# Kernel tuning notes

Hardware: AMD Instinct MI355X
Metric: run time of the kernel (lower is better)

## Reference

```python
import jax, jax.numpy as jnp
import numpy as np
from jax import lax

B, L, E, H, VOCAB = 32, 64, 1024, 128, 32000


def setup_inputs() -> dict:
    key = jax.random.key(0)
    ks = jax.random.split(key, 8)
    return {
        "sent": jax.random.randint(ks[0], (B, L), 0, VOCAB),
        "init_c": jax.random.normal(ks[1], (B, H), jnp.float32),
        "init_h": jax.random.normal(ks[2], (B, H), jnp.float32),
        "enc_output": jax.random.normal(ks[3], (B, E, H), jnp.float32),
        "w_emb": jax.random.normal(ks[4], (VOCAB, H), jnp.float32) * 0.02,
        "w_lstm": jax.random.normal(ks[5], (2 * H, 4 * H), jnp.float32) * 0.05,
        "w_soft": jax.random.normal(ks[6], (H, VOCAB), jnp.float32) * 0.05,
        "V": jax.random.normal(ks[7], (2 * H, H), jnp.float32) * 0.05,
    }


def reference(sent, init_c, init_h, enc_output, w_emb, w_lstm, w_soft, V):
    h_dim = init_h.shape[-1]
    x_emb = w_emb[sent]                       # (B, L, H) embedding lookup
    # Split additive-attention matrix: concat(enc, h) @ V == enc @ V_e + h @ V_h
    V_e, V_h = V[:h_dim], V[h_dim:]           # (H, H) each
    enc_proj = enc_output @ V_e               # (B, E, H), precomputed once

    def step(carry, x_t):
        c, h = carry
        # LSTM cell: gates from concat(x, h) @ w_lstm
        gates = jnp.concatenate([x_t, h], axis=-1) @ w_lstm   # (B, 4H)
        i, f, o, g = jnp.split(gates, 4, axis=-1)
        c_new = jax.nn.sigmoid(f) * c + jax.nn.sigmoid(i) * jnp.tanh(g)
        h_new = jax.nn.sigmoid(o) * jnp.tanh(c_new)           # (B, H)
        # Bahdanau additive attention over encoder states
        att = jnp.tanh(enc_proj + (h_new @ V_h)[:, None, :])  # (B, E, H)
        scores = att.sum(axis=-1)                              # (B, E)
        alpha = jax.nn.softmax(scores, axis=-1)                # (B, E)
        context = jnp.einsum('be,beh->bh', alpha, enc_output)  # (B, H)
        h_out = context                                        # attended hidden
        return (c_new, h_out), (h_out, alpha)

    (c_fin, h_fin), (hs, alphas) = lax.scan(step, (init_c, init_h),
                                            jnp.transpose(x_emb, (1, 0, 2)))
    hs = jnp.transpose(hs, (1, 0, 2))          # (B, L, H)
    alphas = jnp.transpose(alphas, (1, 0, 2))  # (B, L, E)
    logits = hs @ w_soft                       # (B, L, vocab)
    return logits, c_fin, h_fin, alphas
```

## Files before the change

### kernel.cpp

```cpp
#include <hip/hip_runtime.h>
#include <hip/hip_bf16.h>

#define BB 32
#define LL 64
#define EE 1024
#define HH 128
#define VV 32000

typedef unsigned short u16;
typedef unsigned long long u64;
typedef __attribute__((ext_vector_type(8))) short bf16x8;
typedef __attribute__((ext_vector_type(8))) unsigned short u16x8;
typedef __attribute__((ext_vector_type(4))) float f32x4;

#define LOG2E 1.4426950408889634f
#define C2T   2.8853900817779268f

#define OFF_C ((size_t)BB * LL * VV)
#define OFF_H (OFF_C + (size_t)BB * HH)
#define OFF_A (OFF_H + (size_t)BB * HH)

#define WS_ENCT 0
#define WS_HS   ((size_t)16777216)
#define WS_XE   ((size_t)17301504)
#define WS_GX   ((size_t)18350080)
#define WS_PAY  ((size_t)22544384)
#define WS_DFL  ((size_t)23076864)
#define WS_NEED ((size_t)23076868)

#define PAY_WORDS (32 * 8 * 2 * 130)

__device__ __forceinline__ float bf2f(u16 u) {
    union { unsigned int i; float f; } v; v.i = ((unsigned int)u) << 16; return v.f;
}
__device__ __forceinline__ u16 f2bf(float f) {
    union { float f; unsigned int i; } v; v.f = f;
    unsigned int x = v.i;
    return (u16)((x + 0x7FFFu + ((x >> 16) & 1u)) >> 16);
}
__device__ __forceinline__ float ldf(const void* p, size_t i, int f32) {
    if (f32) return ((const float*)p)[i];
    return bf2f(((const u16*)p)[i]);
}
__device__ __forceinline__ void stout(void* p, size_t i, float v, int f32) {
    if (f32) ((float*)p)[i] = v;
    else ((u16*)p)[i] = f2bf(v);
}
__device__ __forceinline__ float sigm(float x) {
    return __builtin_amdgcn_rcpf(1.f + __builtin_amdgcn_exp2f(-x * LOG2E));
}
__device__ __forceinline__ float tanh_fast(float x) {
    return 1.f - 2.f * __builtin_amdgcn_rcpf(__builtin_amdgcn_exp2f(x * C2T) + 1.f);
}

__global__ void detect_kernel(const unsigned int* __restrict__ w, int* __restrict__ flag)
{
    if (threadIdx.x == 0 && blockIdx.x == 0) {
        int cnt = 0;
        for (int i = 0; i < 256; ++i) {
            float a = fabsf(bf2f((u16)(w[i] & 0xFFFFu)));
            if (a > 1e-4f && a < 0.5f) ++cnt;
        }
        *flag = (cnt > 128) ? 1 : 0;
    }
}

__global__ __launch_bounds__(256) void reset_kernel(u64* __restrict__ pay)
{
    int i = blockIdx.x * 256 + threadIdx.x;
    if (i < PAY_WORDS)
        pay[i] = 0ull;
}

__global__ __launch_bounds__(256) void gather_kernel(
    const int* __restrict__ sent, const void* __restrict__ w_emb,
    float* __restrict__ xe, const int* __restrict__ flagp)
{
    int isf32 = !flagp[0];
    int i = blockIdx.x * 256 + threadIdx.x;
    int row = i >> 7, h = i & 127;
    int id = sent[row];
    xe[(size_t)row * HH + h] = ldf(w_emb, (size_t)id * HH + h, isf32);
}

__global__ __launch_bounds__(256) void gatesx2_kernel(
    const float* __restrict__ xe, const void* __restrict__ w_lstm,
    float* __restrict__ gx, const int* __restrict__ flagp)
{
    int isf32 = !flagp[0];
    int row0 = blockIdx.x * 16;
    int tid = threadIdx.x;
    __shared__ float xr[16][128];
    for (int i = tid; i < 2048; i += 256)
        xr[i >> 7][i & 127] = xe[(size_t)(row0 + (i >> 7)) * HH + (i & 127)];
    __syncthreads();
    int c0 = tid, c1 = tid + 256;
    float a0[16], a1[16];
    #pragma unroll
    for (int r = 0; r < 16; ++r) { a0[r] = 0.f; a1[r] = 0.f; }
    for (int kk = 0; kk < 128; ++kk) {
        float w0, w1;
        if (isf32) {
            w0 = ((const float*)w_lstm)[(size_t)kk * 512 + c0];
            w1 = ((const float*)w_lstm)[(size_t)kk * 512 + c1];
        } else {
            w0 = bf2f(((const u16*)w_lstm)[(size_t)kk * 512 + c0]);
            w1 = bf2f(((const u16*)w_lstm)[(size_t)kk * 512 + c1]);
        }
        #pragma unroll
        for (int r = 0; r < 16; ++r) {
            a0[r] += xr[r][kk] * w0;
            a1[r] += xr[r][kk] * w1;
        }
    }
    #pragma unroll
    for (int r = 0; r < 16; ++r) {
        gx[(size_t)(row0 + r) * 512 + c0] = a0[r];
        gx[(size_t)(row0 + r) * 512 + c1] = a1[r];
    }
}

__global__ __launch_bounds__(1024) void transpose_wsoft(
    const void* __restrict__ w_soft, u16* __restrict__ wT, const int* __restrict__ flagp)
{
    int isf32 = !flagp[0];
    __shared__ u16 tile[32][33];
    int n0 = blockIdx.x * 32;
    int k0 = blockIdx.y * 32;
    int tx = threadIdx.x & 31, ty = threadIdx.x >> 5;
    tile[ty][tx] = f2bf(ldf(w_soft, (size_t)(k0 + ty) * VV + n0 + tx, isf32));
    __syncthreads();
    wT[(size_t)(n0 + ty) * HH + k0 + tx] = tile[tx][ty];
}

__global__ __launch_bounds__(256) void encproj_kernel(
    const void* __restrict__ enc_out, const void* __restrict__ V,
    float* __restrict__ encT, const int* __restrict__ flagp)
{
    int isf32 = !flagp[0];
    __shared__ float ve[HH][HH];
    int b = blockIdx.y;
    int e0 = blockIdx.x * 64;
    int tid = threadIdx.x;
    for (int i = tid; i < HH * HH; i += 256)
        ve[i >> 7][i & 127] = ldf(V, i, isf32);
    __syncthreads();
    int e = e0 + (tid & 63);
    int hb = (tid >> 6) * 32;
    size_t rowbase = ((size_t)b * EE + e) * HH;
    float acc[32];
    #pragma unroll
    for (int i = 0; i < 32; ++i) acc[i] = 0.f;
    for (int k0 = 0; k0 < HH; k0 += 16) {
        float ef[16];
        #pragma unroll
        for (int i = 0; i < 16; ++i) ef[i] = ldf(enc_out, rowbase + k0 + i, isf32);
        #pragma unroll
        for (int hh = 0; hh < 32; ++hh) {
            float a = acc[hh];
            #pragma unroll
            for (int kk = 0; kk < 16; ++kk)
                a += ef[kk] * ve[k0 + kk][hb + hh];
            acc[hh] = a;
        }
    }
    float* outp = encT + ((size_t)b * HH) * EE + e;
    #pragma unroll
    for (int hh = 0; hh < 32; ++hh)
        outp[(size_t)(hb + hh) * EE] = acc[hh] * C2T;
}

__global__ __launch_bounds__(1024, 4) void scan_kernel(
    const void* __restrict__ init_c, const void* __restrict__ init_h,
    const void* __restrict__ enc_out, const void* __restrict__ w_lstm,
    const void* __restrict__ V, const float* __restrict__ encTg,
    const float* __restrict__ gx, u16* __restrict__ hs_bf,
    void* __restrict__ out, u64* __restrict__ pay,
    const int* __restrict__ flagp)
{
    const int isf32 = !flagp[0];
    const int bid = blockIdx.x;
    const int b = bid & 31, k = bid >> 5;
    const int tid = threadIdx.x;

    __shared__ float encTl[128][128];
    __shared__ float harr[128], cst[128], hnew[128], hvC[128];
    __shared__ float gp[2][512];
    __shared__ float dred[8][128];
    __shared__ float sc[128], Ul[128];
    __shared__ float exch[8][130];
    __shared__ float redw[2], redw2[2];
    __shared__ float m_s, s_s;

    for (int i = tid; i < 128 * 128; i += 1024) {
        int h = i >> 7, e = i & 127;
        encTl[h][e] = encTg[(size_t)(b * 128 + h) * EE + k * 128 + e];
    }
    if (tid < 128) {
        cst[tid]  = ldf(init_c, (size_t)b * HH + tid, isf32);
        harr[tid] = ldf(init_h, (size_t)b * HH + tid, isf32);
    }
    __syncthreads();

    u64* mypay = pay + (size_t)(b * 8 + k) * 2 * 130;

    for (int t = 0; t < LL; ++t) {
        {
            int col = tid & 511, half = tid >> 9;
            float acc = 0.f;
            if (isf32) {
                const float* wcol = (const float*)w_lstm + (size_t)(HH + half * 64) * 512 + col;
                #pragma unroll 4
                for (int kk = 0; kk < 64; ++kk)
                    acc += harr[half * 64 + kk] * wcol[(size_t)kk * 512];
            } else {
                const u16* wcol = (const u16*)w_lstm + (size_t)(HH + half * 64) * 512 + col;
                #pragma unroll 4
                for (int kk = 0; kk < 64; ++kk)
                    acc += harr[half * 64 + kk] * bf2f(wcol[(size_t)kk * 512]);
            }
            gp[half][col] = acc;
        }
        __syncthreads();
        if (tid < 128) {
            const float* gxr = gx + (size_t)(b * LL + t) * 512;
            float gi = gxr[tid]       + gp[0][tid]       + gp[1][tid];
            float gf = gxr[128 + tid] + gp[0][128 + tid] + gp[1][128 + tid];
            float go = gxr[256 + tid] + gp[0][256 + tid] + gp[1][256 + tid];
            float gg = gxr[384 + tid] + gp[0][384 + tid] + gp[1][384 + tid];
            float c_new = sigm(gf) * cst[tid] + sigm(gi) * tanh_fast(gg);
            cst[tid] = c_new;
            hnew[tid] = sigm(go) * tanh_fast(c_new);
        }
        __syncthreads();
        {
            int h = tid & 127, jc = tid >> 7;
            float p = 0.f;
            if (isf32) {
                const float* vp = (const float*)V + (size_t)(HH + jc * 16) * HH + h;
                #pragma unroll
                for (int j = 0; j < 16; ++j)
                    p += hnew[jc * 16 + j] * vp[(size_t)j * HH];
            } else {
                const u16* vp = (const u16*)V + (size_t)(HH + jc * 16) * HH + h;
                #pragma unroll
                for (int j = 0; j < 16; ++j)
                    p += hnew[jc * 16 + j] * bf2f(vp[(size_t)j * HH]);
            }
            dred[jc][h] = p;
        }
        __syncthreads();
        if (tid < 128) {
            float v = 0.f;
            #pragma unroll
            for (int s = 0; s < 8; ++s) v += dred[s][tid];
            hvC[tid] = v * C2T;
        }
        __syncthreads();
        {
            int e = tid & 127, hc = tid >> 7;
            float sumr = 0.f;
            #pragma unroll
            for (int j = 0; j < 16; ++j) {
                int h = hc * 16 + j;
                float a = encTl[h][e] + hvC[h];
                sumr += __builtin_amdgcn_rcpf(__builtin_amdgcn_exp2f(a) + 1.f);
            }
            dred[hc][e] = sumr;
        }
        __syncthreads();
        float s_e = 0.f, p_reg = 0.f;
        if (tid < 128) {
            float sr = 0.f;
            #pragma unroll
            for (int s = 0; s < 8; ++s) sr += dred[s][tid];
            s_e = 128.f - 2.f * sr;
            float m = s_e;
            #pragma unroll
            for (int off = 32; off; off >>= 1) m = fmaxf(m, __shfl_xor(m, off));
            if ((tid & 63) == 0) redw[tid >> 6] = m;
        }
        __syncthreads();
        if (tid < 128) {
            float mloc = fmaxf(redw[0], redw[1]);
            p_reg = __builtin_amdgcn_exp2f((s_e - mloc) * LOG2E);
            sc[tid] = p_reg;
            float s = p_reg;
            #pragma unroll
            for (int off = 32; off; off >>= 1) s += __shfl_xor(s, off);
            if ((tid & 63) == 0) redw2[tid >> 6] = s;
            if (tid == 0) m_s = mloc;
        }
        __syncthreads();
        if (tid == 0) s_s = redw2[0] + redw2[1];
        {
            int h = tid & 127, ec = tid >> 7;
            float p = 0.f;
            if (isf32) {
                const float* eb = (const float*)enc_out +
                    ((size_t)b * EE + k * 128 + ec * 16) * HH + h;
                #pragma unroll
                for (int j = 0; j < 16; ++j)
                    p += sc[ec * 16 + j] * eb[(size_t)j * HH];
            } else {
                const u16* eb = (const u16*)enc_out +
                    ((size_t)b * EE + k * 128 + ec * 16) * HH + h;
                #pragma unroll
                for (int j = 0; j < 16; ++j)
                    p += sc[ec * 16 + j] * bf2f(eb[(size_t)j * HH]);
            }
            __syncthreads();
            dred[ec][h] = p;
        }
        __syncthreads();
        if (tid < 128) {
            float v = 0.f;
            #pragma unroll
            for (int s = 0; s < 8; ++s) v += dred[s][tid];
            Ul[tid] = v;
        }
        __syncthreads();
        {
            u64* pp = mypay + (size_t)(t & 1) * 130;
            if (tid < 130) {
                float val = (tid < 128) ? Ul[tid] : ((tid == 128) ? m_s : s_s);
                union { float f; unsigned int u; } cv; cv.f = val;
                u64 w = ((u64)(unsigned int)(t + 1) << 32) | (u64)cv.u;
                __hip_atomic_store(&pp[tid], w, __ATOMIC_RELAXED, __HIP_MEMORY_SCOPE_AGENT);
            }
        }
        if (tid < 910) {
            int qq = tid / 130;
            int q = qq + (qq >= k ? 1 : 0);
            int idx = tid - qq * 130;
            const u64* qp = pay + ((size_t)(b * 8 + q) * 2 + (t & 1)) * 130 + idx;
            unsigned int want = (unsigned int)(t + 1);
            u64 w = __hip_atomic_load(qp, __ATOMIC_RELAXED, __HIP_MEMORY_SCOPE_AGENT);
            int cnt = 0;
            while ((unsigned int)(w >> 32) != want) {
                __builtin_amdgcn_s_sleep(2);
                w = __hip_atomic_load(qp, __ATOMIC_RELAXED, __HIP_MEMORY_SCOPE_AGENT);
                if (++cnt > (1 << 20)) break;
            }
            union { unsigned int u; float f; } cv; cv.u = (unsigned int)(w & 0xFFFFFFFFu);
            exch[q][idx] = cv.f;
        }
        if (tid < 130) {
            float val = (tid < 128) ? Ul[tid] : ((tid == 128) ? m_s : s_s);
            exch[k][tid] = val;
        }
        __syncthreads();
        if (tid < 128) {
            float M = exch[0][128];
            #pragma unroll
            for (int q = 1; q < 8; ++q) M = fmaxf(M, exch[q][128]);
            float St = 0.f, ch = 0.f;
            #pragma unroll
            for (int q = 0; q < 8; ++q) {
                float w = __builtin_amdgcn_exp2f((exch[q][128] - M) * LOG2E);
                St += w * exch[q][129];
                ch += w * exch[q][tid];
            }
            float rS = __builtin_amdgcn_rcpf(St);
            float ctx = ch * rS;
            harr[tid] = ctx;
            float al = sc[tid] * __builtin_amdgcn_exp2f((m_s - M) * LOG2E) * rS;
            stout(out, OFF_A + (size_t)(b * LL + t) * EE + k * 128 + tid, al, isf32);
            if (k == 0) {
                hs_bf[(size_t)(b * LL + t) * HH + tid] = f2bf(ctx);
                if (t == LL - 1) {
                    stout(out, OFF_H + (size_t)b * HH + tid, ctx, isf32);
                    stout(out, OFF_C + (size_t)b * HH + tid, cst[tid], isf32);
                }
            }
        }
        __syncthreads();
    }
}

__global__ __launch_bounds__(256) void logits_gemm(
    const u16* __restrict__ hs, const u16* __restrict__ wT,
    void* __restrict__ out, const int* __restrict__ flagp)
{
    int isf32 = !flagp[0];
    int n0 = blockIdx.x * 32;
    int m0 = (blockIdx.y * 4 + (threadIdx.x >> 6)) * 32;
    int lane = threadIdx.x & 63;
    int lr = lane & 15, lh = lane >> 4;
    f32x4 acc00 = {0.f, 0.f, 0.f, 0.f}, acc01 = acc00, acc10 = acc00, acc11 = acc00;
    const u16* a0p = hs + (size_t)(m0 + lr) * HH + lh * 8;
    const u16* a1p = a0p + (size_t)16 * HH;
    const u16* b0p = wT + (size_t)(n0 + lr) * HH + lh * 8;
    const u16* b1p = b0p + (size_t)16 * HH;
    #pragma unroll
    for (int ks = 0; ks < 4; ++ks) {
        bf16x8 a0 = *(const bf16x8*)(a0p + ks * 32);
        bf16x8 a1 = *(const bf16x8*)(a1p + ks * 32);
        bf16x8 b0 = *(const bf16x8*)(b0p + ks * 32);
        bf16x8 b1 = *(const bf16x8*)(b1p + ks * 32);
        acc00 = __builtin_amdgcn_mfma_f32_16x16x32_bf16(a0, b0, acc00, 0, 0, 0);
        acc01 = __builtin_amdgcn_mfma_f32_16x16x32_bf16(a0, b1, acc01, 0, 0, 0);
        acc10 = __builtin_amdgcn_mfma_f32_16x16x32_bf16(a1, b0, acc10, 0, 0, 0);
        acc11 = __builtin_amdgcn_mfma_f32_16x16x32_bf16(a1, b1, acc11, 0, 0, 0);
    }
    size_t base0 = (size_t)(m0 + lh * 4) * VV + n0;
    size_t base1 = (size_t)(m0 + 16 + lh * 4) * VV + n0;
    #pragma unroll
    for (int r = 0; r < 4; ++r) {
        stout(out, base0 + (size_t)r * VV + lr,      acc00[r], isf32);
        stout(out, base0 + (size_t)r * VV + 16 + lr, acc01[r], isf32);
        stout(out, base1 + (size_t)r * VV + lr,      acc10[r], isf32);
        stout(out, base1 + (size_t)r * VV + 16 + lr, acc11[r], isf32);
    }
}

extern "C" void kernel_launch(void* const* d_in, const int* in_sizes, int n_in,
                              void* d_out, int out_size, void* d_ws, size_t ws_size,
                              hipStream_t stream)
{
    (void)in_sizes; (void)n_in; (void)out_size;
    if (ws_size < WS_NEED) return;

    const int* sent     = (const int*)d_in[0];
    const void* init_c  = d_in[1];
    const void* init_h  = d_in[2];
    const void* enc_out = d_in[3];
    const void* w_emb   = d_in[4];
    const void* w_lstm  = d_in[5];
    const void* w_soft  = d_in[6];
    const void* V       = d_in[7];

    char* ws = (char*)d_ws;
    float* encT  = (float*)(ws + WS_ENCT);
    u16*   wT    = (u16*)(ws + WS_ENCT);
    u16*   hs    = (u16*)(ws + WS_HS);
    float* xe    = (float*)(ws + WS_XE);
    float* gx    = (float*)(ws + WS_GX);
    u64*   pay   = (u64*)(ws + WS_PAY);
    int*   dflag = (int*)(ws + WS_DFL);

    hipLaunchKernelGGL(detect_kernel, dim3(1), dim3(64), 0, stream,
                       (const unsigned int*)w_emb, dflag);
    hipLaunchKernelGGL(reset_kernel, dim3((PAY_WORDS + 255) / 256), dim3(256), 0, stream, pay);
    hipLaunchKernelGGL(gather_kernel, dim3(1024), dim3(256), 0, stream, sent, w_emb, xe, dflag);
    hipLaunchKernelGGL(gatesx2_kernel, dim3(128), dim3(256), 0, stream, xe, w_lstm, gx, dflag);
    hipLaunchKernelGGL(encproj_kernel, dim3(16, BB), dim3(256), 0, stream, enc_out, V, encT, dflag);

    {
        const void* a0 = init_c; const void* a1 = init_h; const void* a2 = enc_out;
        const void* a3 = w_lstm; const void* a4 = V; const float* a5 = encT;
        const float* a6 = gx; u16* a7 = hs; void* a8 = d_out;
        u64* a9 = pay; const int* a10 = dflag;
        void* args[] = {&a0, &a1, &a2, &a3, &a4, &a5, &a6, &a7, &a8, &a9, &a10};
        hipLaunchCooperativeKernel(scan_kernel, dim3(256), dim3(1024), args, 0, stream);
    }

    hipLaunchKernelGGL(transpose_wsoft, dim3(VV / 32, 4), dim3(1024), 0, stream, w_soft, wT, dflag);
    hipLaunchKernelGGL(logits_gemm, dim3(VV / 32, 16), dim3(256), 0, stream, hs, wT, d_out, dflag);
}
```

Measured before the change: 892.0 us.

## Keep recurrent weights in registers and fuse small setup kernels

```diff
diff --git a/kernel.cpp b/kernel.cpp
--- a/kernel.cpp
+++ b/kernel.cpp
@@ -22,7 +22,6 @@
 
 #define WS_ENCT 0
 #define WS_HS   ((size_t)16777216)
-#define WS_XE   ((size_t)17301504)
 #define WS_GX   ((size_t)18350080)
 #define WS_PAY  ((size_t)22544384)
 #define WS_DFL  ((size_t)23076864)
@@ -53,46 +52,36 @@
     return 1.f - 2.f * __builtin_amdgcn_rcpf(__builtin_amdgcn_exp2f(x * C2T) + 1.f);
 }
 
-__global__ void detect_kernel(const unsigned int* __restrict__ w, int* __restrict__ flag)
-{
-    if (threadIdx.x == 0 && blockIdx.x == 0) {
-        int cnt = 0;
-        for (int i = 0; i < 256; ++i) {
-            float a = fabsf(bf2f((u16)(w[i] & 0xFFFFu)));
-            if (a > 1e-4f && a < 0.5f) ++cnt;
-        }
-        *flag = (cnt > 128) ? 1 : 0;
-    }
-}
-
-__global__ __launch_bounds__(256) void reset_kernel(u64* __restrict__ pay)
+__global__ __launch_bounds__(256) void resetdetect_kernel(
+    u64* __restrict__ pay, const unsigned int* __restrict__ w, int* __restrict__ flag)
 {
     int i = blockIdx.x * 256 + threadIdx.x;
     if (i < PAY_WORDS)
         pay[i] = 0ull;
-}
-
-__global__ __launch_bounds__(256) void gather_kernel(
+    if (i == 0) {
+        int cnt = 0;
+        for (int j = 0; j < 256; ++j) {
+            float a = fabsf(bf2f((u16)(w[j] & 0xFFFFu)));
+            if (a > 1e-4f && a < 0.5f) ++cnt;
+        }
+        *flag = (cnt > 128) ? 1 : 0;
+    }
+}
+
+__global__ __launch_bounds__(256) void gatesx3_kernel(
     const int* __restrict__ sent, const void* __restrict__ w_emb,
-    float* __restrict__ xe, const int* __restrict__ flagp)
-{
-    int isf32 = !flagp[0];
-    int i = blockIdx.x * 256 + threadIdx.x;
-    int row = i >> 7, h = i & 127;
-    int id = sent[row];
-    xe[(size_t)row * HH + h] = ldf(w_emb, (size_t)id * HH + h, isf32);
-}
-
-__global__ __launch_bounds__(256) void gatesx2_kernel(
-    const float* __restrict__ xe, const void* __restrict__ w_lstm,
-    float* __restrict__ gx, const int* __restrict__ flagp)
+    const void* __restrict__ w_lstm, float* __restrict__ gx,
+    const int* __restrict__ flagp)
 {
     int isf32 = !flagp[0];
     int row0 = blockIdx.x * 16;
     int tid = threadIdx.x;
     __shared__ float xr[16][128];
-    for (int i = tid; i < 2048; i += 256)
-        xr[i >> 7][i & 127] = xe[(size_t)(row0 + (i >> 7)) * HH + (i & 127)];
+    for (int i = tid; i < 2048; i += 256) {
+        int r = i >> 7, col = i & 127;
+        int id = sent[row0 + r];
+        xr[r][col] = ldf(w_emb, (size_t)id * HH + col, isf32);
+    }
     __syncthreads();
     int c0 = tid, c1 = tid + 256;
     float a0[16], a1[16];
@@ -170,7 +159,7 @@
         outp[(size_t)(hb + hh) * EE] = acc[hh] * C2T;
 }
 
-__global__ __launch_bounds__(1024, 4) void scan_kernel(
+__global__ __launch_bounds__(1024, 2) void scan_kernel(
     const void* __restrict__ init_c, const void* __restrict__ init_h,
     const void* __restrict__ enc_out, const void* __restrict__ w_lstm,
     const void* __restrict__ V, const float* __restrict__ encTg,
@@ -192,6 +181,17 @@
     __shared__ float redw[2], redw2[2];
     __shared__ float m_s, s_s;
 
+    const int colA = tid & 511, halfA = tid >> 9;
+    float wreg[64];
+    #pragma unroll
+    for (int kk = 0; kk < 64; ++kk)
+        wreg[kk] = ldf(w_lstm, (size_t)(HH + halfA * 64 + kk) * 512 + colA, isf32);
+    const int hC = tid & 127, jcC = tid >> 7;
+    float vreg[16];
+    #pragma unroll
+    for (int j = 0; j < 16; ++j)
+        vreg[j] = ldf(V, (size_t)(HH + jcC * 16 + j) * HH + hC, isf32);
+
     for (int i = tid; i < 128 * 128; i += 1024) {
         int h = i >> 7, e = i & 127;
         encTl[h][e] = encTg[(size_t)(b * 128 + h) * EE + k * 128 + e];
@@ -205,49 +205,35 @@
     u64* mypay = pay + (size_t)(b * 8 + k) * 2 * 130;
 
     for (int t = 0; t < LL; ++t) {
+        float g0 = 0.f, g1 = 0.f, g2 = 0.f, g3 = 0.f;
+        if (tid < 128) {
+            const float* gxr = gx + (size_t)(b * LL + t) * 512;
+            g0 = gxr[tid]; g1 = gxr[128 + tid]; g2 = gxr[256 + tid]; g3 = gxr[384 + tid];
+        }
         {
-            int col = tid & 511, half = tid >> 9;
             float acc = 0.f;
-            if (isf32) {
-                const float* wcol = (const float*)w_lstm + (size_t)(HH + half * 64) * 512 + col;
-                #pragma unroll 4
-                for (int kk = 0; kk < 64; ++kk)
-                    acc += harr[half * 64 + kk] * wcol[(size_t)kk * 512];
-            } else {
-                const u16* wcol = (const u16*)w_lstm + (size_t)(HH + half * 64) * 512 + col;
-                #pragma unroll 4
-                for (int kk = 0; kk < 64; ++kk)
-                    acc += harr[half * 64 + kk] * bf2f(wcol[(size_t)kk * 512]);
-            }
-            gp[half][col] = acc;
-        }
-        __syncthreads();
-        if (tid < 128) {
-            const float* gxr = gx + (size_t)(b * LL + t) * 512;
-            float gi = gxr[tid]       + gp[0][tid]       + gp[1][tid];
-            float gf = gxr[128 + tid] + gp[0][128 + tid] + gp[1][128 + tid];
-            float go = gxr[256 + tid] + gp[0][256 + tid] + gp[1][256 + tid];
-            float gg = gxr[384 + tid] + gp[0][384 + tid] + gp[1][384 + tid];
+            #pragma unroll
+            for (int kk = 0; kk < 64; ++kk)
+                acc += harr[halfA * 64 + kk] * wreg[kk];
+            gp[halfA][colA] = acc;
+        }
+        __syncthreads();
+        if (tid < 128) {
+            float gi = g0 + gp[0][tid]       + gp[1][tid];
+            float gf = g1 + gp[0][128 + tid] + gp[1][128 + tid];
+            float go = g2 + gp[0][256 + tid] + gp[1][256 + tid];
+            float gg = g3 + gp[0][384 + tid] + gp[1][384 + tid];
             float c_new = sigm(gf) * cst[tid] + sigm(gi) * tanh_fast(gg);
             cst[tid] = c_new;
             hnew[tid] = sigm(go) * tanh_fast(c_new);
         }
         __syncthreads();
         {
-            int h = tid & 127, jc = tid >> 7;
             float p = 0.f;
-            if (isf32) {
-                const float* vp = (const float*)V + (size_t)(HH + jc * 16) * HH + h;
-                #pragma unroll
-                for (int j = 0; j < 16; ++j)
-                    p += hnew[jc * 16 + j] * vp[(size_t)j * HH];
-            } else {
-                const u16* vp = (const u16*)V + (size_t)(HH + jc * 16) * HH + h;
-                #pragma unroll
-                for (int j = 0; j < 16; ++j)
-                    p += hnew[jc * 16 + j] * bf2f(vp[(size_t)j * HH]);
-            }
-            dred[jc][h] = p;
+            #pragma unroll
+            for (int j = 0; j < 16; ++j)
+                p += hnew[jcC * 16 + j] * vreg[j];
+            dred[jcC][hC] = p;
         }
         __syncthreads();
         if (tid < 128) {
@@ -434,16 +420,14 @@
     float* encT  = (float*)(ws + WS_ENCT);
     u16*   wT    = (u16*)(ws + WS_ENCT);
     u16*   hs    = (u16*)(ws + WS_HS);
-    float* xe    = (float*)(ws + WS_XE);
     float* gx    = (float*)(ws + WS_GX);
     u64*   pay   = (u64*)(ws + WS_PAY);
     int*   dflag = (int*)(ws + WS_DFL);
 
-    hipLaunchKernelGGL(detect_kernel, dim3(1), dim3(64), 0, stream,
-                       (const unsigned int*)w_emb, dflag);
-    hipLaunchKernelGGL(reset_kernel, dim3((PAY_WORDS + 255) / 256), dim3(256), 0, stream, pay);
-    hipLaunchKernelGGL(gather_kernel, dim3(1024), dim3(256), 0, stream, sent, w_emb, xe, dflag);
-    hipLaunchKernelGGL(gatesx2_kernel, dim3(128), dim3(256), 0, stream, xe, w_lstm, gx, dflag);
+    hipLaunchKernelGGL(resetdetect_kernel, dim3((PAY_WORDS + 255) / 256), dim3(256), 0, stream,
+                       pay, (const unsigned int*)w_emb, dflag);
+    hipLaunchKernelGGL(gatesx3_kernel, dim3(128), dim3(256), 0, stream,
+                       sent, w_emb, w_lstm, gx, dflag);
     hipLaunchKernelGGL(encproj_kernel, dim3(16, BB), dim3(256), 0, stream, enc_out, V, encT, dflag);
 
     {
```

Result: slower. 944.5 us (+5.9%).
